# Kernel tuning notes

Hardware: AMD Instinct MI355X
Metric: run time of the kernel (lower is better)

The kernel has to match this reference:

```python
import jax, jax.numpy as jnp
import numpy as np

EP, T1, N, H, OUT = 512, 1024, 128, 256, 64  # epcho, t_1(=bs), input_size, hidden_size, output_size


def setup_inputs() -> dict:
    key = jax.random.key(0)
    ks = jax.random.split(key, 9)
    w = lambda k, shape: jax.random.normal(k, shape, dtype=jnp.float32) * 0.05
    return dict(
        input=jax.random.normal(ks[0], (EP, T1, N), dtype=jnp.float32),
        hidden=jnp.zeros((1, T1, H), dtype=jnp.float32),  # (n_layers, bs, hidden)
        W_ih=w(ks[1], (3 * H, N)),   # GRU weight_ih_l0 (r,z,n gates stacked)
        W_hh=w(ks[2], (3 * H, H)),   # GRU weight_hh_l0
        b_ih=w(ks[3], (3 * H,)),
        b_hh=w(ks[4], (3 * H,)),
        W_hr=w(ks[5], (N, H)),
        b_hr=w(ks[6], (N,)),
        W_reg=w(ks[7], (OUT, T1)),
        b_reg=w(ks[8], (OUT,)),
    )


def reference(input, hidden, W_ih, W_hh, b_ih, b_hh, W_hr, b_hr, W_reg, b_reg):
    # Sequential GRU recurrence over the epcho axis; each step is a GRUCell with
    # batch = t_1 and seq_len = 1 (exactly what the torch loop computes).
    h0 = hidden[0]  # (T1, H) -- single layer

    def step(h, x):  # h: (T1, H), x: (T1, N)
        gi = x @ W_ih.T + b_ih            # (T1, 3H)
        gh = h @ W_hh.T + b_hh            # (T1, 3H)
        i_r, i_z, i_n = jnp.split(gi, 3, axis=-1)
        h_r, h_z, h_n = jnp.split(gh, 3, axis=-1)
        r = jax.nn.sigmoid(i_r + h_r)
        z = jax.nn.sigmoid(i_z + h_z)
        n_t = jnp.tanh(i_n + r * h_n)
        h_new = (1.0 - z) * n_t + z * h   # (T1, H)
        out = (h_new @ W_hr.T + b_hr).T
        return h_new, out

    _, outputs = jax.lax.scan(step, h0, input)  # (EP, N, T1)
    return outputs @ W_reg.T + b_reg            # (EP, N, OUT)
```

## Files before the change

### kernel.cpp

```cpp
#include <hip/hip_runtime.h>
#include <hip/hip_bf16.h>

#define EPN  512
#define T1N  1024
#define NIN  128
#define HSN  256
#define OUTN 64
#define NBLK 256
#define NTHR 256

typedef __attribute__((ext_vector_type(8))) short bf16x8;
typedef __attribute__((ext_vector_type(4))) short bf16x4;
typedef __attribute__((ext_vector_type(4))) float f32x4;
typedef __attribute__((ext_vector_type(4))) unsigned int u32x4;
typedef unsigned long long u64;

struct KArgs {
  const float *x, *h0, *W_ih, *W_hh, *b_ih, *b_hh, *W_hr, *b_hr, *W_reg, *b_reg;
  float *out;
  ushort *hb;
  ushort *Ppart;
  float *Pbuf;
  float *Sreg;
  unsigned int *hflags;
  unsigned int *pflags;
};

__device__ __forceinline__ float sigm(float v) { return 1.f / (1.f + __expf(-v)); }
__device__ __forceinline__ float tanh_fast(float v) { return 2.f / (1.f + __expf(-2.f * v)) - 1.f; }
__device__ __forceinline__ short f2bf(float f) {
  return (short)__builtin_bit_cast(ushort, __float2bfloat16(f));
}
__device__ __forceinline__ bf16x8 cvt8(f32x4 a, f32x4 b) {
  bf16x8 r;
  r[0]=f2bf(a[0]); r[1]=f2bf(a[1]); r[2]=f2bf(a[2]); r[3]=f2bf(a[3]);
  r[4]=f2bf(b[0]); r[5]=f2bf(b[1]); r[6]=f2bf(b[2]); r[7]=f2bf(b[3]);
  return r;
}

__device__ __forceinline__ bf16x8 ld16h_sc(const ushort* p) {
  bf16x8 v; asm volatile("global_load_dwordx4 %0, %1, off sc0 sc1" : "=v"(v) : "v"(p)); return v;
}
__device__ __forceinline__ f32x4 ld16f_sc(const float* p) {
  f32x4 v; asm volatile("global_load_dwordx4 %0, %1, off sc0 sc1" : "=v"(v) : "v"(p)); return v;
}
__device__ __forceinline__ u32x4 ld16u_sc(const unsigned int* p) {
  u32x4 v; asm volatile("global_load_dwordx4 %0, %1, off sc0 sc1" : "=v"(v) : "v"(p)); return v;
}
__device__ __forceinline__ unsigned int ld2h_sc(const ushort* p) {
  unsigned int v; asm volatile("global_load_ushort %0, %1, off sc0 sc1" : "=v"(v) : "v"(p)); return v;
}
__device__ __forceinline__ u64 at8(ushort* p, bf16x4 v) {
  return __hip_atomic_exchange((u64*)p, __builtin_bit_cast(u64, v),
                               __ATOMIC_RELAXED, __HIP_MEMORY_SCOPE_SYSTEM);
}
__device__ __forceinline__ u64 at4(float* p, float v) {
  return (u64)__hip_atomic_exchange((unsigned int*)p, __builtin_bit_cast(unsigned int, v),
                                    __ATOMIC_RELAXED, __HIP_MEMORY_SCOPE_SYSTEM);
}
#define SINK(x) asm volatile("" :: "v"(x))
__device__ __forceinline__ void st4f_sc(float* p, float v) {
  asm volatile("global_store_dword %0, %1, off sc0 sc1" :: "v"(p), "v"(v) : "memory");
}
__device__ __forceinline__ void st4u_sc(unsigned int* p, unsigned int v) {
  asm volatile("global_store_dword %0, %1, off sc0 sc1" :: "v"(p), "v"(v) : "memory");
}
__device__ __forceinline__ f32x4 ld16f(const float* p) {
  f32x4 v; asm volatile("global_load_dwordx4 %0, %1, off" : "=v"(v) : "v"(p)); return v;
}
#define WAITV0 do { asm volatile("s_waitcnt vmcnt(0)" ::: "memory"); \
                    __builtin_amdgcn_sched_barrier(0); } while (0)

__device__ __forceinline__ unsigned int min4(u32x4 v) {
  unsigned int m = v[0];
  m = v[1] < m ? v[1] : m; m = v[2] < m ? v[2] : m; m = v[3] < m ? v[3] : m;
  return m;
}
template<int SLP>
__device__ __forceinline__ void pollflags(const unsigned int* f, int nquad,
                                          unsigned int target, int lane) {
  int spins = 0;
  for (;;) {
    unsigned int m = 0xFFFFFFFFu;
    if (lane < nquad) m = min4(ld16u_sc(f + lane * 4));
    asm volatile("s_waitcnt vmcnt(0)" ::: "memory");
    if (__all((int)(m >= target))) break;
    if (++spins > (1 << 17)) break;
    __builtin_amdgcn_s_sleep(SLP);
  }
}

#define MFMA(A,B,C) __builtin_amdgcn_mfma_f32_16x16x32_bf16(A, B, C, 0, 0, 0)

__global__ void gru_setup(KArgs a) {
  const int gtid = blockIdx.x * blockDim.x + threadIdx.x;
  const int gsz = gridDim.x * blockDim.x;
  if (gtid < 512) { if (gtid < 256) a.hflags[gtid] = 0; else a.pflags[gtid - 256] = 0; }
  for (int i = gtid; i < T1N * HSN; i += gsz)
    a.hb[i] = __builtin_bit_cast(ushort, __float2bfloat16(a.h0[i]));
  if (gtid < OUTN) {
    float ssum = 0.f; const float* wr = a.W_reg + (size_t)gtid * T1N;
    for (int t = 0; t < T1N; ++t) ssum += wr[t];
    a.Sreg[gtid] = ssum;
  }
}

__global__ __launch_bounds__(NTHR, 1) void gru12(KArgs a) {
  const int bid = blockIdx.x, tid = threadIdx.x;

  const int tgrp = bid & 15, cgrp = bid >> 4;
  const int t0 = tgrp * 64, c0 = cgrp * 16;

  __shared__ __align__(16) short WtL[64 * 80];
  __shared__ __align__(16) short hT [16 * 80];
  __shared__ float cpart[256];

  {
    int o = tid >> 2, seg = tid & 3;
    const float* wr = a.W_reg + (size_t)o * T1N + t0 + seg * 16;
    bf16x8 p0, p1;
    #pragma unroll
    for (int j = 0; j < 8; ++j) p0[j] = f2bf(wr[j]);
    #pragma unroll
    for (int j = 0; j < 8; ++j) p1[j] = f2bf(wr[8 + j]);
    *(bf16x8*)&WtL[o * 80 + seg * 16]     = p0;
    *(bf16x8*)&WtL[o * 80 + seg * 16 + 8] = p1;
  }
  __syncthreads();

  const int lane = tid & 63, wv_ = tid >> 6;
  const int cl = lane & 15, kg = lane >> 4;
  const int tb = t0 + wv_ * 16;
  const int c  = c0 + cl;
  const float bR  = a.b_ih[c] + a.b_hh[c];
  const float bZ  = a.b_ih[HSN + c] + a.b_hh[HSN + c];
  const float bIN = a.b_ih[2*HSN + c];
  const float bHN = a.b_hh[2*HSN + c];

  bf16x8 whR[8], whZ[8], whN[8];
  #pragma unroll
  for (int ks = 0; ks < 8; ++ks) {
    const float* pr = a.W_hh + (size_t)(0*HSN + c) * HSN + ks * 32 + kg * 8;
    const float* pz = a.W_hh + (size_t)(1*HSN + c) * HSN + ks * 32 + kg * 8;
    const float* pn = a.W_hh + (size_t)(2*HSN + c) * HSN + ks * 32 + kg * 8;
    whR[ks] = cvt8(*(const f32x4*)pr, *(const f32x4*)(pr + 4));
    whZ[ks] = cvt8(*(const f32x4*)pz, *(const f32x4*)(pz + 4));
    whN[ks] = cvt8(*(const f32x4*)pn, *(const f32x4*)(pn + 4));
  }
  bf16x8 wxR[4], wxZ[4], wxN[4];
  #pragma unroll
  for (int ks = 0; ks < 4; ++ks) {
    const float* pr = a.W_ih + (size_t)(0*HSN + c) * NIN + ks * 32 + kg * 8;
    const float* pz = a.W_ih + (size_t)(1*HSN + c) * NIN + ks * 32 + kg * 8;
    const float* pn = a.W_ih + (size_t)(2*HSN + c) * NIN + ks * 32 + kg * 8;
    wxR[ks] = cvt8(*(const f32x4*)pr, *(const f32x4*)(pr + 4));
    wxZ[ks] = cvt8(*(const f32x4*)pz, *(const f32x4*)(pz + 4));
    wxN[ks] = cvt8(*(const f32x4*)pn, *(const f32x4*)(pn + 4));
  }

  const int n0 = bid >> 1, oh = (bid & 1) * 32;
  const int oo = tid & 31, part = tid >> 5;
  f32x4 whr[8];
  #pragma unroll
  for (int j = 0; j < 8; ++j) whr[j] = *(const f32x4*)&a.W_hr[(size_t)n0 * HSN + part * 32 + j * 4];
  const float cb = a.b_hr[n0];
  const float sregv = a.Sreg[oh + oo];
  const float bregv = a.b_reg[oh + oo];

  float hp[4];
  #pragma unroll
  for (int r = 0; r < 4; ++r) hp[r] = a.h0[(size_t)(tb + kg * 4 + r) * HSN + c];

  f32x4 giR = {0,0,0,0}, giZ = {0,0,0,0}, giN = {0,0,0,0};
  {
    const float* xrow = a.x + (size_t)(tb + cl) * NIN + kg * 8;
    #pragma unroll
    for (int ks = 0; ks < 4; ++ks) {
      f32x4 x0 = *(const f32x4*)(xrow + ks * 32);
      f32x4 x1 = *(const f32x4*)(xrow + ks * 32 + 4);
      bf16x8 af = cvt8(x0, x1);
      giR = MFMA(af, wxR[ks], giR); giZ = MFMA(af, wxZ[ks], giZ); giN = MFMA(af, wxN[ks], giN);
    }
  }

  for (int s = 0; s < EPN + 4; ++s) {
    const ushort* hb_r = a.hb + (size_t)(s & 1) * (T1N * HSN);
    ushort*       hb_w = a.hb + (size_t)((s + 1) & 1) * (T1N * HSN);

    if (wv_ == 0) {
      if (s >= 2) pollflags<2>(a.pflags, 64, (unsigned)(s - 1), lane);
    } else if (wv_ == 1) {
      if (s >= 1 && s < EPN) pollflags<1>(a.hflags + tgrp * 16, 4, (unsigned)s, lane);
    }
    __syncthreads();

    bf16x8 hfr[8];
    if (s < EPN) {
      const ushort* hrow = hb_r + (size_t)(tb + cl) * HSN + kg * 8;
      #pragma unroll
      for (int ks = 0; ks < 8; ++ks) hfr[ks] = ld16h_sc(hrow + ks * 32);
    }
    unsigned int rv[16];
    const bool hasR = (s >= 2 && s < EPN + 2);
    if (tid < 64 && hasR) {
      const ushort* pp = a.Ppart + (size_t)((s - 2) & 3) * (16 * 16384) + bid * 64 + tid;
      #pragma unroll
      for (int j = 0; j < 16; ++j) rv[j] = ld2h_sc(pp + (size_t)j * 16384);
    }
    f32x4 cv[8];
    if (s >= 4) {
      const float* pb = a.Pbuf + (size_t)((s - 4) & 3) * 16384 + (size_t)(oh + oo) * 256 + part * 32;
      #pragma unroll
      for (int j = 0; j < 8; ++j) cv[j] = ld16f_sc(pb + j * 4);
    }
    f32x4 xa[4], xb[4];
    const bool hasX = (s + 1 < EPN);
    if (hasX) {
      const float* xrow = a.x + ((size_t)(s + 1) * T1N + tb + cl) * NIN + kg * 8;
      #pragma unroll
      for (int ks = 0; ks < 4; ++ks) {
        xa[ks] = ld16f(xrow + ks * 32);
        xb[ks] = ld16f(xrow + ks * 32 + 4);
      }
    }
    WAITV0;

    if (s < EPN) {
      f32x4 accR = {0,0,0,0}, accZ = {0,0,0,0}, accN = {0,0,0,0};
      #pragma unroll
      for (int ks = 0; ks < 8; ++ks) {
        accR = MFMA(hfr[ks], whR[ks], accR);
        accZ = MFMA(hfr[ks], whZ[ks], accZ);
        accN = MFMA(hfr[ks], whN[ks], accN);
      }
      bf16x4 hpk;
      #pragma unroll
      for (int r = 0; r < 4; ++r) {
        float rr = sigm(accR[r] + giR[r] + bR);
        float zz = sigm(accZ[r] + giZ[r] + bZ);
        float nn = tanh_fast(giN[r] + bIN + rr * (accN[r] + bHN));
        float hn = (1.f - zz) * nn + zz * hp[r];
        hp[r] = hn;
        hpk[r] = f2bf(hn);
      }
      *(bf16x4*)&hT[cl * 80 + wv_ * 16 + kg * 4] = hpk;
    }
    __syncthreads();

    if (s < EPN) {
      int th = tid >> 2, c4 = (tid & 3) * 4;
      bf16x4 hpk2;
      #pragma unroll
      for (int j = 0; j < 4; ++j) hpk2[j] = hT[(c4 + j) * 80 + th];
      u64 hold = at8(hb_w + (size_t)(t0 + th) * HSN + c0 + c4, hpk2);
      SINK(hold);
    }
    WAITV0;
    __syncthreads();
    if (s < EPN && tid == 0) st4u_sc(a.hflags + tgrp * 16 + cgrp, (unsigned)(s + 1));

    u64 pdum = 0;
    if (s < EPN) {
      f32x4 pacc = {0,0,0,0};
      #pragma unroll
      for (int ks = 0; ks < 2; ++ks) {
        bf16x8 pa = *(const bf16x8*)&hT[cl * 80 + ks * 32 + kg * 8];
        bf16x8 pb = *(const bf16x8*)&WtL[(wv_ * 16 + cl) * 80 + ks * 32 + kg * 8];
        pacc = MFMA(pa, pb, pacc);
      }
      bf16x4 pk;
      #pragma unroll
      for (int r = 0; r < 4; ++r) pk[r] = f2bf(pacc[r]);
      pdum ^= at8(a.Ppart + ((size_t)(s & 3) * 16 + tgrp) * 16384 + (size_t)(wv_ * 16 + cl) * 256 + c0 + kg * 4, pk);
    }
    if (tid < 64 && hasR) {
      float sum = 0.f;
      #pragma unroll
      for (int j = 0; j < 16; ++j) sum += __builtin_bit_cast(float, rv[j] << 16);
      pdum ^= at4(a.Pbuf + (size_t)((s - 2) & 3) * 16384 + bid * 64 + tid, sum);
    }
    if (s >= 4) {
      float cacc = 0.f;
      #pragma unroll
      for (int j = 0; j < 8; ++j)
        cacc += whr[j][0]*cv[j][0] + whr[j][1]*cv[j][1] + whr[j][2]*cv[j][2] + whr[j][3]*cv[j][3];
      cpart[part * 32 + oo] = cacc;
    }
    f32x4 giR2 = {0,0,0,0}, giZ2 = {0,0,0,0}, giN2 = {0,0,0,0};
    if (hasX) {
      #pragma unroll
      for (int ks = 0; ks < 4; ++ks) {
        bf16x8 af = cvt8(xa[ks], xb[ks]);
        giR2 = MFMA(af, wxR[ks], giR2); giZ2 = MFMA(af, wxZ[ks], giZ2); giN2 = MFMA(af, wxN[ks], giN2);
      }
    }
    giR = giR2; giZ = giZ2; giN = giN2;

    SINK(pdum);
    WAITV0;
    __syncthreads();
    if (s >= 4 && tid < 32) {
      float v = cb * sregv + bregv;
      #pragma unroll
      for (int p = 0; p < 8; ++p) v += cpart[p * 32 + tid];
      st4f_sc(a.out + ((size_t)(s - 4) * NIN + n0) * OUTN + oh + tid, v);
    }
    if (tid == 0) st4u_sc(a.pflags + bid, (unsigned)(s + 1));
  }
}

extern "C" void kernel_launch(void* const* d_in, const int* in_sizes, int n_in,
                              void* d_out, int out_size, void* d_ws, size_t ws_size,
                              hipStream_t stream) {
  KArgs a;
  a.x     = (const float*)d_in[0];
  a.h0    = (const float*)d_in[1];
  a.W_ih  = (const float*)d_in[2];
  a.W_hh  = (const float*)d_in[3];
  a.b_ih  = (const float*)d_in[4];
  a.b_hh  = (const float*)d_in[5];
  a.W_hr  = (const float*)d_in[6];
  a.b_hr  = (const float*)d_in[7];
  a.W_reg = (const float*)d_in[8];
  a.b_reg = (const float*)d_in[9];
  a.out   = (float*)d_out;

  char* w = (char*)d_ws;
  a.hflags = (unsigned int*)w; w += 256 * 4;
  a.pflags = (unsigned int*)w; w += 256 * 4;
  a.Sreg   = (float*)w;        w += 256;
  a.hb     = (ushort*)w;       w += (size_t)2 * T1N * HSN * 2;
  a.Pbuf   = (float*)w;        w += (size_t)4 * 16384 * 4;
  a.Ppart  = (ushort*)w;       w += (size_t)4 * 16 * 16384 * 2;

  hipLaunchKernelGGL(gru_setup, dim3(64), dim3(NTHR), 0, stream, a);
  hipLaunchKernelGGL(gru12, dim3(NBLK), dim3(NTHR), 0, stream, a);
}
```

Before: 4.363 ms.

## Warp-specialize GRU kernel into recurrence and projection/regression thread groups

The block grows to 512 threads and is split into two roles. The first 256 threads only run the hidden-state recurrence. The other 256 compute the next step's input projection into double-buffered shared memory (giL) and do the partial-product and regression reductions, delayed by one extra step. This takes x loads, input MFMAs and output work off the serial critical path. In exchange there are more threads per block, a higher register-pressure risk from the launch bounds, and shared barriers that couple the two roles every step.

```diff
diff --git a/kernel.cpp b/kernel.cpp
--- a/kernel.cpp
+++ b/kernel.cpp
@@ -7,7 +7,7 @@
 #define HSN  256
 #define OUTN 64
 #define NBLK 256
-#define NTHR 256
+#define NTHR 512
 
 typedef __attribute__((ext_vector_type(8))) short bf16x8;
 typedef __attribute__((ext_vector_type(4))) short bf16x4;
@@ -70,6 +70,10 @@
 }
 #define WAITV0 do { asm volatile("s_waitcnt vmcnt(0)" ::: "memory"); \
                     __builtin_amdgcn_sched_barrier(0); } while (0)
+#define BAR do { asm volatile("s_waitcnt lgkmcnt(0)" ::: "memory"); \
+                 __builtin_amdgcn_s_barrier(); \
+                 asm volatile("" ::: "memory"); \
+                 __builtin_amdgcn_sched_barrier(0); } while (0)
 
 __device__ __forceinline__ unsigned int min4(u32x4 v) {
   unsigned int m = v[0];
@@ -105,207 +109,222 @@
   }
 }
 
-__global__ __launch_bounds__(NTHR, 1) void gru12(KArgs a) {
+__global__ __launch_bounds__(NTHR, 2) void gru13(KArgs a) {
   const int bid = blockIdx.x, tid = threadIdx.x;
-
   const int tgrp = bid & 15, cgrp = bid >> 4;
   const int t0 = tgrp * 64, c0 = cgrp * 16;
 
   __shared__ __align__(16) short WtL[64 * 80];
-  __shared__ __align__(16) short hT [16 * 80];
+  __shared__ __align__(16) short hT2[2][16 * 80];
+  __shared__ __align__(16) f32x4 giL[2][3][256];
   __shared__ float cpart[256];
 
-  {
-    int o = tid >> 2, seg = tid & 3;
-    const float* wr = a.W_reg + (size_t)o * T1N + t0 + seg * 16;
-    bf16x8 p0, p1;
+  if (tid < 256) {
+    const int lane = tid & 63, wv_ = tid >> 6;
+    const int cl = lane & 15, kg = lane >> 4;
+    const int tb = t0 + wv_ * 16;
+    const int c  = c0 + cl;
+    const float bR  = a.b_ih[c] + a.b_hh[c];
+    const float bZ  = a.b_ih[HSN + c] + a.b_hh[HSN + c];
+    const float bIN = a.b_ih[2*HSN + c];
+    const float bHN = a.b_hh[2*HSN + c];
+
+    bf16x8 whR[8], whZ[8], whN[8];
     #pragma unroll
-    for (int j = 0; j < 8; ++j) p0[j] = f2bf(wr[j]);
+    for (int ks = 0; ks < 8; ++ks) {
+      const float* pr = a.W_hh + (size_t)(0*HSN + c) * HSN + ks * 32 + kg * 8;
+      const float* pz = a.W_hh + (size_t)(1*HSN + c) * HSN + ks * 32 + kg * 8;
+      const float* pn = a.W_hh + (size_t)(2*HSN + c) * HSN + ks * 32 + kg * 8;
+      whR[ks] = cvt8(*(const f32x4*)pr, *(const f32x4*)(pr + 4));
+      whZ[ks] = cvt8(*(const f32x4*)pz, *(const f32x4*)(pz + 4));
+      whN[ks] = cvt8(*(const f32x4*)pn, *(const f32x4*)(pn + 4));
+    }
+    float hp[4];
     #pragma unroll
-    for (int j = 0; j < 8; ++j) p1[j] = f2bf(wr[8 + j]);
-    *(bf16x8*)&WtL[o * 80 + seg * 16]     = p0;
-    *(bf16x8*)&WtL[o * 80 + seg * 16 + 8] = p1;
-  }
-  __syncthreads();
-
-  const int lane = tid & 63, wv_ = tid >> 6;
-  const int cl = lane & 15, kg = lane >> 4;
-  const int tb = t0 + wv_ * 16;
-  const int c  = c0 + cl;
-  const float bR  = a.b_ih[c] + a.b_hh[c];
-  const float bZ  = a.b_ih[HSN + c] + a.b_hh[HSN + c];
-  const float bIN = a.b_ih[2*HSN + c];
-  const float bHN = a.b_hh[2*HSN + c];
-
-  bf16x8 whR[8], whZ[8], whN[8];
-  #pragma unroll
-  for (int ks = 0; ks < 8; ++ks) {
-    const float* pr = a.W_hh + (size_t)(0*HSN + c) * HSN + ks * 32 + kg * 8;
-    const float* pz = a.W_hh + (size_t)(1*HSN + c) * HSN + ks * 32 + kg * 8;
-    const float* pn = a.W_hh + (size_t)(2*HSN + c) * HSN + ks * 32 + kg * 8;
-    whR[ks] = cvt8(*(const f32x4*)pr, *(const f32x4*)(pr + 4));
-    whZ[ks] = cvt8(*(const f32x4*)pz, *(const f32x4*)(pz + 4));
-    whN[ks] = cvt8(*(const f32x4*)pn, *(const f32x4*)(pn + 4));
-  }
-  bf16x8 wxR[4], wxZ[4], wxN[4];
-  #pragma unroll
-  for (int ks = 0; ks < 4; ++ks) {
-    const float* pr = a.W_ih + (size_t)(0*HSN + c) * NIN + ks * 32 + kg * 8;
-    const float* pz = a.W_ih + (size_t)(1*HSN + c) * NIN + ks * 32 + kg * 8;
-    const float* pn = a.W_ih + (size_t)(2*HSN + c) * NIN + ks * 32 + kg * 8;
-    wxR[ks] = cvt8(*(const f32x4*)pr, *(const f32x4*)(pr + 4));
-    wxZ[ks] = cvt8(*(const f32x4*)pz, *(const f32x4*)(pz + 4));
-    wxN[ks] = cvt8(*(const f32x4*)pn, *(const f32x4*)(pn + 4));
-  }
-
-  const int n0 = bid >> 1, oh = (bid & 1) * 32;
-  const int oo = tid & 31, part = tid >> 5;
-  f32x4 whr[8];
-  #pragma unroll
-  for (int j = 0; j < 8; ++j) whr[j] = *(const f32x4*)&a.W_hr[(size_t)n0 * HSN + part * 32 + j * 4];
-  const float cb = a.b_hr[n0];
-  const float sregv = a.Sreg[oh + oo];
-  const float bregv = a.b_reg[oh + oo];
-
-  float hp[4];
-  #pragma unroll
-  for (int r = 0; r < 4; ++r) hp[r] = a.h0[(size_t)(tb + kg * 4 + r) * HSN + c];
-
-  f32x4 giR = {0,0,0,0}, giZ = {0,0,0,0}, giN = {0,0,0,0};
-  {
-    const float* xrow = a.x + (size_t)(tb + cl) * NIN + kg * 8;
+    for (int r = 0; r < 4; ++r) hp[r] = a.h0[(size_t)(tb + kg * 4 + r) * HSN + c];
+
+    for (int s = 0; s < EPN + 5; ++s) {
+      if (tid < 64 && s >= 1 && s < EPN)
+        pollflags<1>(a.hflags + tgrp * 16, 4, (unsigned)s, tid);
+      BAR;
+
+      if (s < EPN) {
+        bf16x8 hfr[8];
+        const ushort* hrow = a.hb + (size_t)(s & 1) * (T1N * HSN)
+                           + (size_t)(tb + cl) * HSN + kg * 8;
+        #pragma unroll
+        for (int ks = 0; ks < 8; ++ks) hfr[ks] = ld16h_sc(hrow + ks * 32);
+        WAITV0;
+        f32x4 accR = {0,0,0,0}, accZ = {0,0,0,0}, accN = {0,0,0,0};
+        #pragma unroll
+        for (int ks = 0; ks < 8; ++ks) {
+          accR = MFMA(hfr[ks], whR[ks], accR);
+          accZ = MFMA(hfr[ks], whZ[ks], accZ);
+          accN = MFMA(hfr[ks], whN[ks], accN);
+        }
+        f32x4 g0 = giL[s & 1][0][tid];
+        f32x4 g1 = giL[s & 1][1][tid];
+        f32x4 g2 = giL[s & 1][2][tid];
+        bf16x4 hpk;
+        #pragma unroll
+        for (int r = 0; r < 4; ++r) {
+          float rr = sigm(accR[r] + g0[r] + bR);
+          float zz = sigm(accZ[r] + g1[r] + bZ);
+          float nn = tanh_fast(g2[r] + bIN + rr * (accN[r] + bHN));
+          float hn = (1.f - zz) * nn + zz * hp[r];
+          hp[r] = hn;
+          hpk[r] = f2bf(hn);
+        }
+        *(bf16x4*)&hT2[s & 1][cl * 80 + wv_ * 16 + kg * 4] = hpk;
+      }
+      BAR;
+
+      if (s < EPN) {
+        int th = tid >> 2, c4 = (tid & 3) * 4;
+        bf16x4 hpk2;
+        #pragma unroll
+        for (int j = 0; j < 4; ++j) hpk2[j] = hT2[s & 1][(c4 + j) * 80 + th];
+        u64 hold = at8(a.hb + (size_t)((s + 1) & 1) * (T1N * HSN)
+                       + (size_t)(t0 + th) * HSN + c0 + c4, hpk2);
+        SINK(hold);
+      }
+      WAITV0;
+      BAR;
+      if (s < EPN && tid == 0)
+        st4u_sc(a.hflags + tgrp * 16 + cgrp, (unsigned)(s + 1));
+    }
+  } else {
+    const int tp = tid - 256;
+    const int lane = tp & 63, wvp = tp >> 6;
+    const int clp = lane & 15, kgp = lane >> 4;
+    const int tbp = t0 + wvp * 16;
+    const int cp  = c0 + clp;
+
+    bf16x8 wxR[4], wxZ[4], wxN[4];
     #pragma unroll
     for (int ks = 0; ks < 4; ++ks) {
-      f32x4 x0 = *(const f32x4*)(xrow + ks * 32);
-      f32x4 x1 = *(const f32x4*)(xrow + ks * 32 + 4);
-      bf16x8 af = cvt8(x0, x1);
-      giR = MFMA(af, wxR[ks], giR); giZ = MFMA(af, wxZ[ks], giZ); giN = MFMA(af, wxN[ks], giN);
-    }
-  }
-
-  for (int s = 0; s < EPN + 4; ++s) {
-    const ushort* hb_r = a.hb + (size_t)(s & 1) * (T1N * HSN);
-    ushort*       hb_w = a.hb + (size_t)((s + 1) & 1) * (T1N * HSN);
-
-    if (wv_ == 0) {
-      if (s >= 2) pollflags<2>(a.pflags, 64, (unsigned)(s - 1), lane);
-    } else if (wv_ == 1) {
-      if (s >= 1 && s < EPN) pollflags<1>(a.hflags + tgrp * 16, 4, (unsigned)s, lane);
-    }
-    __syncthreads();
-
-    bf16x8 hfr[8];
-    if (s < EPN) {
-      const ushort* hrow = hb_r + (size_t)(tb + cl) * HSN + kg * 8;
+      const float* pr = a.W_ih + (size_t)(0*HSN + cp) * NIN + ks * 32 + kgp * 8;
+      const float* pz = a.W_ih + (size_t)(1*HSN + cp) * NIN + ks * 32 + kgp * 8;
+      const float* pn = a.W_ih + (size_t)(2*HSN + cp) * NIN + ks * 32 + kgp * 8;
+      wxR[ks] = cvt8(*(const f32x4*)pr, *(const f32x4*)(pr + 4));
+      wxZ[ks] = cvt8(*(const f32x4*)pz, *(const f32x4*)(pz + 4));
+      wxN[ks] = cvt8(*(const f32x4*)pn, *(const f32x4*)(pn + 4));
+    }
+    {
+      int o = tp >> 2, seg = tp & 3;
+      const float* wr = a.W_reg + (size_t)o * T1N + t0 + seg * 16;
+      bf16x8 p0, p1;
       #pragma unroll
-      for (int ks = 0; ks < 8; ++ks) hfr[ks] = ld16h_sc(hrow + ks * 32);
-    }
-    unsigned int rv[16];
-    const bool hasR = (s >= 2 && s < EPN + 2);
-    if (tid < 64 && hasR) {
-      const ushort* pp = a.Ppart + (size_t)((s - 2) & 3) * (16 * 16384) + bid * 64 + tid;
+      for (int j = 0; j < 8; ++j) p0[j] = f2bf(wr[j]);
       #pragma unroll
-      for (int j = 0; j < 16; ++j) rv[j] = ld2h_sc(pp + (size_t)j * 16384);
-    }
-    f32x4 cv[8];
-    if (s >= 4) {
-      const float* pb = a.Pbuf + (size_t)((s - 4) & 3) * 16384 + (size_t)(oh + oo) * 256 + part * 32;
-      #pragma unroll
-      for (int j = 0; j < 8; ++j) cv[j] = ld16f_sc(pb + j * 4);
-    }
-    f32x4 xa[4], xb[4];
-    const bool hasX = (s + 1 < EPN);
-    if (hasX) {
-      const float* xrow = a.x + ((size_t)(s + 1) * T1N + tb + cl) * NIN + kg * 8;
+      for (int j = 0; j < 8; ++j) p1[j] = f2bf(wr[8 + j]);
+      *(bf16x8*)&WtL[o * 80 + seg * 16]     = p0;
+      *(bf16x8*)&WtL[o * 80 + seg * 16 + 8] = p1;
+    }
+    const int n0 = bid >> 1, oh = (bid & 1) * 32;
+    const int oo = tp & 31, part = tp >> 5;
+    f32x4 whr[8];
+    #pragma unroll
+    for (int j = 0; j < 8; ++j) whr[j] = *(const f32x4*)&a.W_hr[(size_t)n0 * HSN + part * 32 + j * 4];
+    const float cb    = a.b_hr[n0];
+    const float sregv = a.Sreg[oh + oo];
+    const float bregv = a.b_reg[oh + oo];
+
+    {
+      const float* xrow = a.x + (size_t)(tbp + clp) * NIN + kgp * 8;
+      f32x4 r0 = {0,0,0,0}, r1 = {0,0,0,0}, r2 = {0,0,0,0};
       #pragma unroll
       for (int ks = 0; ks < 4; ++ks) {
-        xa[ks] = ld16f(xrow + ks * 32);
-        xb[ks] = ld16f(xrow + ks * 32 + 4);
-      }
-    }
-    WAITV0;
-
-    if (s < EPN) {
-      f32x4 accR = {0,0,0,0}, accZ = {0,0,0,0}, accN = {0,0,0,0};
-      #pragma unroll
-      for (int ks = 0; ks < 8; ++ks) {
-        accR = MFMA(hfr[ks], whR[ks], accR);
-        accZ = MFMA(hfr[ks], whZ[ks], accZ);
-        accN = MFMA(hfr[ks], whN[ks], accN);
-      }
-      bf16x4 hpk;
-      #pragma unroll
-      for (int r = 0; r < 4; ++r) {
-        float rr = sigm(accR[r] + giR[r] + bR);
-        float zz = sigm(accZ[r] + giZ[r] + bZ);
-        float nn = tanh_fast(giN[r] + bIN + rr * (accN[r] + bHN));
-        float hn = (1.f - zz) * nn + zz * hp[r];
-        hp[r] = hn;
-        hpk[r] = f2bf(hn);
-      }
-      *(bf16x4*)&hT[cl * 80 + wv_ * 16 + kg * 4] = hpk;
-    }
-    __syncthreads();
-
-    if (s < EPN) {
-      int th = tid >> 2, c4 = (tid & 3) * 4;
-      bf16x4 hpk2;
-      #pragma unroll
-      for (int j = 0; j < 4; ++j) hpk2[j] = hT[(c4 + j) * 80 + th];
-      u64 hold = at8(hb_w + (size_t)(t0 + th) * HSN + c0 + c4, hpk2);
-      SINK(hold);
-    }
-    WAITV0;
-    __syncthreads();
-    if (s < EPN && tid == 0) st4u_sc(a.hflags + tgrp * 16 + cgrp, (unsigned)(s + 1));
-
-    u64 pdum = 0;
-    if (s < EPN) {
-      f32x4 pacc = {0,0,0,0};
-      #pragma unroll
-      for (int ks = 0; ks < 2; ++ks) {
-        bf16x8 pa = *(const bf16x8*)&hT[cl * 80 + ks * 32 + kg * 8];
-        bf16x8 pb = *(const bf16x8*)&WtL[(wv_ * 16 + cl) * 80 + ks * 32 + kg * 8];
-        pacc = MFMA(pa, pb, pacc);
-      }
-      bf16x4 pk;
-      #pragma unroll
-      for (int r = 0; r < 4; ++r) pk[r] = f2bf(pacc[r]);
-      pdum ^= at8(a.Ppart + ((size_t)(s & 3) * 16 + tgrp) * 16384 + (size_t)(wv_ * 16 + cl) * 256 + c0 + kg * 4, pk);
-    }
-    if (tid < 64 && hasR) {
-      float sum = 0.f;
-      #pragma unroll
-      for (int j = 0; j < 16; ++j) sum += __builtin_bit_cast(float, rv[j] << 16);
-      pdum ^= at4(a.Pbuf + (size_t)((s - 2) & 3) * 16384 + bid * 64 + tid, sum);
-    }
-    if (s >= 4) {
-      float cacc = 0.f;
-      #pragma unroll
-      for (int j = 0; j < 8; ++j)
-        cacc += whr[j][0]*cv[j][0] + whr[j][1]*cv[j][1] + whr[j][2]*cv[j][2] + whr[j][3]*cv[j][3];
-      cpart[part * 32 + oo] = cacc;
-    }
-    f32x4 giR2 = {0,0,0,0}, giZ2 = {0,0,0,0}, giN2 = {0,0,0,0};
-    if (hasX) {
-      #pragma unroll
-      for (int ks = 0; ks < 4; ++ks) {
-        bf16x8 af = cvt8(xa[ks], xb[ks]);
-        giR2 = MFMA(af, wxR[ks], giR2); giZ2 = MFMA(af, wxZ[ks], giZ2); giN2 = MFMA(af, wxN[ks], giN2);
-      }
-    }
-    giR = giR2; giZ = giZ2; giN = giN2;
-
-    SINK(pdum);
-    WAITV0;
-    __syncthreads();
-    if (s >= 4 && tid < 32) {
-      float v = cb * sregv + bregv;
-      #pragma unroll
-      for (int p = 0; p < 8; ++p) v += cpart[p * 32 + tid];
-      st4f_sc(a.out + ((size_t)(s - 4) * NIN + n0) * OUTN + oh + tid, v);
-    }
-    if (tid == 0) st4u_sc(a.pflags + bid, (unsigned)(s + 1));
+        f32x4 x0 = *(const f32x4*)(xrow + ks * 32);
+        f32x4 x1 = *(const f32x4*)(xrow + ks * 32 + 4);
+        bf16x8 af = cvt8(x0, x1);
+        r0 = MFMA(af, wxR[ks], r0); r1 = MFMA(af, wxZ[ks], r1); r2 = MFMA(af, wxN[ks], r2);
+      }
+      giL[0][0][tp] = r0; giL[0][1][tp] = r1; giL[0][2][tp] = r2;
+    }
+
+    for (int s = 0; s < EPN + 5; ++s) {
+      if (tp < 64 && s >= 2)
+        pollflags<2>(a.pflags, 64, (unsigned)(s - 1), tp);
+      BAR;
+
+      unsigned int rv[16];
+      const bool hasR = (s >= 3 && s <= EPN + 2);
+      if (tp < 64 && hasR) {
+        const ushort* pp = a.Ppart + (size_t)((s - 3) & 3) * (16 * 16384) + bid * 64 + tp;
+        #pragma unroll
+        for (int j = 0; j < 16; ++j) rv[j] = ld2h_sc(pp + (size_t)j * 16384);
+      }
+      f32x4 cv[8];
+      const bool hasC = (s >= 5 && s < EPN + 5);
+      if (hasC) {
+        const float* pb = a.Pbuf + (size_t)((s - 5) & 3) * 16384 + (size_t)(oh + oo) * 256 + part * 32;
+        #pragma unroll
+        for (int j = 0; j < 8; ++j) cv[j] = ld16f_sc(pb + j * 4);
+      }
+      f32x4 xa[4], xb[4];
+      const bool hasX = (s + 1 < EPN);
+      if (hasX) {
+        const float* xrow = a.x + ((size_t)(s + 1) * T1N + tbp + clp) * NIN + kgp * 8;
+        #pragma unroll
+        for (int ks = 0; ks < 4; ++ks) {
+          xa[ks] = ld16f(xrow + ks * 32);
+          xb[ks] = ld16f(xrow + ks * 32 + 4);
+        }
+      }
+      WAITV0;
+
+      u64 pdum = 0;
+      if (s >= 1 && s <= EPN) {
+        f32x4 pacc = {0,0,0,0};
+        #pragma unroll
+        for (int ks = 0; ks < 2; ++ks) {
+          bf16x8 pa = *(const bf16x8*)&hT2[(s - 1) & 1][clp * 80 + ks * 32 + kgp * 8];
+          bf16x8 pb = *(const bf16x8*)&WtL[(wvp * 16 + clp) * 80 + ks * 32 + kgp * 8];
+          pacc = MFMA(pa, pb, pacc);
+        }
+        bf16x4 pk;
+        #pragma unroll
+        for (int r = 0; r < 4; ++r) pk[r] = f2bf(pacc[r]);
+        pdum ^= at8(a.Ppart + ((size_t)((s - 1) & 3) * 16 + tgrp) * 16384
+                    + (size_t)(wvp * 16 + clp) * 256 + c0 + kgp * 4, pk);
+      }
+      BAR;
+
+      if (tp < 64 && hasR) {
+        float sum = 0.f;
+        #pragma unroll
+        for (int j = 0; j < 16; ++j) sum += __builtin_bit_cast(float, rv[j] << 16);
+        pdum ^= at4(a.Pbuf + (size_t)((s - 3) & 3) * 16384 + bid * 64 + tp, sum);
+      }
+      if (hasC) {
+        float cacc = 0.f;
+        #pragma unroll
+        for (int j = 0; j < 8; ++j)
+          cacc += whr[j][0]*cv[j][0] + whr[j][1]*cv[j][1] + whr[j][2]*cv[j][2] + whr[j][3]*cv[j][3];
+        cpart[tp] = cacc;
+      }
+      if (hasX) {
+        f32x4 r0 = {0,0,0,0}, r1 = {0,0,0,0}, r2 = {0,0,0,0};
+        #pragma unroll
+        for (int ks = 0; ks < 4; ++ks) {
+          bf16x8 af = cvt8(xa[ks], xb[ks]);
+          r0 = MFMA(af, wxR[ks], r0); r1 = MFMA(af, wxZ[ks], r1); r2 = MFMA(af, wxN[ks], r2);
+        }
+        giL[(s + 1) & 1][0][tp] = r0; giL[(s + 1) & 1][1][tp] = r1; giL[(s + 1) & 1][2][tp] = r2;
+      }
+      SINK(pdum);
+      WAITV0;
+      BAR;
+
+      if (hasC && tp < 32) {
+        float v = cb * sregv + bregv;
+        #pragma unroll
+        for (int p = 0; p < 8; ++p) v += cpart[p * 32 + tp];
+        st4f_sc(a.out + ((size_t)(s - 5) * NIN + n0) * OUTN + oh + tp, v);
+      }
+      if (tp == 0) st4u_sc(a.pflags + bid, (unsigned)(s + 1));
+    }
   }
 }
 
@@ -333,6 +352,6 @@
   a.Pbuf   = (float*)w;        w += (size_t)4 * 16384 * 4;
   a.Ppart  = (ushort*)w;       w += (size_t)4 * 16 * 16384 * 2;
 
-  hipLaunchKernelGGL(gru_setup, dim3(64), dim3(NTHR), 0, stream, a);
-  hipLaunchKernelGGL(gru12, dim3(NBLK), dim3(NTHR), 0, stream, a);
-}
+  hipLaunchKernelGGL(gru_setup, dim3(64), dim3(256), 0, stream, a);
+  hipLaunchKernelGGL(gru13, dim3(NBLK), dim3(NTHR), 0, stream, a);
+}
```

Measured after the change: 3.840 ms (median of 2 runs). 1.14x faster.
